# Performance work log

Hardware: AMD Instinct MI355X
Metric: run time of the kernel (lower is better)

## Reference

```python
import jax, jax.numpy as jnp
import numpy as np

TEMPERATURE = 0.1

def _l2norm(x):
    # F.normalize(dim=1) with eps clamp
    n = jnp.maximum(jnp.linalg.norm(x, axis=1, keepdims=True), 1e-12)
    return x / n

def _retrieval_metric(s):
    # T=1: position of the diagonal element in each row's descending sort.
    order = jnp.argsort(-s, axis=1)            # [N,N] descending argsort
    rankpos = jnp.argsort(order, axis=1)        # inverse permutation: rank of each column
    pos = jnp.diagonal(rankpos)                 # j such that rank[i][j] == i
    posf = pos.astype(s.dtype)
    r1 = jnp.mean((pos < 1).astype(s.dtype))
    r5 = jnp.mean((pos < 5).astype(s.dtype))
    r10 = jnp.mean((pos < 10).astype(s.dtype))
    mr = jnp.mean(posf)
    return r1, r5, r10, mr

def setup_inputs() -> dict:
    key = jax.random.key(0)
    k1, k2, k3, k4 = jax.random.split(key, 4)
    N, C = 4096, 512
    return {
        'v_feat': jax.random.normal(k1, (N, C), dtype=jnp.float32),
        't_feat': jax.random.normal(k2, (N, C), dtype=jnp.float32),
        'p_v': jax.random.normal(k3, (N, C), dtype=jnp.float32),
        'p_t': jax.random.normal(k4, (N, C), dtype=jnp.float32),
    }

def reference(v_feat, t_feat, p_v, p_t):
    vn = _l2norm(v_feat)
    tn = _l2norm(t_feat)
    pvn = _l2norm(p_v)
    ptn = _l2norm(p_t)
    sv = jnp.einsum('nc,mc->nm', vn, ptn) / TEMPERATURE  # [N,N]
    st = jnp.einsum('nc,mc->nm', tn, pvn) / TEMPERATURE  # [N,N]
    # nominator: scalar logsumexp over both diagonals (2N values)
    nominator = jax.nn.logsumexp(jnp.concatenate([jnp.diagonal(sv), jnp.diagonal(st)], axis=0))
    # denominator: per-row logsumexp over concatenated [N,2N]
    denominator = jax.nn.logsumexp(jnp.concatenate([sv, st], axis=1), axis=1)
    loss = jnp.mean(denominator - nominator)
    # metrics (no-grad path in original)
    v_std = jnp.mean(jnp.std(vn, axis=0, ddof=1))
    t_std = jnp.mean(jnp.std(tn, axis=0, ddof=1))
    pv_std = jnp.mean(jnp.std(pvn, axis=0, ddof=1))
    pt_std = jnp.mean(jnp.std(ptn, axis=0, ddof=1))
    sv_raw = jnp.einsum('nc,mc->nm', vn, ptn)
    st_raw = jnp.einsum('nc,mc->nm', tn, pvn)
    v_r1, v_r5, v_r10, v_mr = _retrieval_metric(sv_raw)
    t_r1, t_r5, t_r10, t_mr = _retrieval_metric(st_raw)
    return (loss, v_std, t_std, pv_std, pt_std,
            v_r1, v_r5, v_r10, v_mr,
            t_r1, t_r5, t_r10, t_mr)
```

## Files before the change

### kernel.cpp

```cpp
#include <hip/hip_runtime.h>
#include <hip/hip_bf16.h>

#define N 4096
#define C 512

typedef __attribute__((ext_vector_type(8))) short bf16x8;
typedef __attribute__((ext_vector_type(8))) short s16x8;
typedef __attribute__((ext_vector_type(4))) float f32x4;

__device__ inline float bf2f(__hip_bfloat16 h) { return __bfloat162float(h); }

__device__ inline void gload16(const void* g, void* l) {
    __builtin_amdgcn_global_load_lds(
        (__attribute__((address_space(1))) void*)(g),
        (__attribute__((address_space(3))) void*)(l),
        16, 0, 0);
}

__global__ __launch_bounds__(256) void k_prep(
    const float* __restrict__ s0, const float* __restrict__ s1f,
    const float* __restrict__ s2f, const float* __restrict__ s3,
    __hip_bfloat16* __restrict__ ws_hi0, long mat_stride,
    float* __restrict__ dv, float* __restrict__ dt,
    float* __restrict__ colsum, float* __restrict__ colsq)
{
    __shared__ float sa[4][512];
    __shared__ float sq[4][512];

    const int b = blockIdx.x;
    const int tid = threadIdx.x;
    const int lane = tid & 63;
    const int w = tid >> 6;

    const int pair = b >> 8;
    const int chunk = b & 255;
    const float* X = pair ? s1f : s0;
    const float* B = pair ? s2f : s3;
    const int mX = pair ? 1 : 0;
    const int mB = pair ? 2 : 3;
    __hip_bfloat16* hiX = ws_hi0 + (long)mX * mat_stride;
    __hip_bfloat16* loX = hiX + (long)N * C;
    __hip_bfloat16* hiB = ws_hi0 + (long)mB * mat_stride;
    __hip_bfloat16* loB = hiB + (long)N * C;
    float* dout = pair ? dt : dv;

    float aX[8], qX[8], aB[8], qB[8];
    for (int e = 0; e < 8; e++) { aX[e] = 0.f; qX[e] = 0.f; aB[e] = 0.f; qB[e] = 0.f; }

    const int row0 = chunk * 16 + w * 4;
    for (int i = 0; i < 4; i++) {
        const int row = row0 + i;
        const float4* x4 = (const float4*)(X + (size_t)row * C);
        const float4* b4 = (const float4*)(B + (size_t)row * C);
        float4 x0 = x4[lane * 2], x1 = x4[lane * 2 + 1];
        float4 b0 = b4[lane * 2], b1 = b4[lane * 2 + 1];

        float ss  = x0.x*x0.x + x0.y*x0.y + x0.z*x0.z + x0.w*x0.w
                  + x1.x*x1.x + x1.y*x1.y + x1.z*x1.z + x1.w*x1.w;
        float ssb = b0.x*b0.x + b0.y*b0.y + b0.z*b0.z + b0.w*b0.w
                  + b1.x*b1.x + b1.y*b1.y + b1.z*b1.z + b1.w*b1.w;
        float dot = x0.x*b0.x + x0.y*b0.y + x0.z*b0.z + x0.w*b0.w
                  + x1.x*b1.x + x1.y*b1.y + x1.z*b1.z + x1.w*b1.w;
        for (int o = 1; o < 64; o <<= 1) {
            ss  += __shfl_xor(ss, o);
            ssb += __shfl_xor(ssb, o);
            dot += __shfl_xor(dot, o);
        }
        float scX = 1.0f / fmaxf(sqrtf(ss), 1e-12f);
        float scB = 1.0f / fmaxf(sqrtf(ssb), 1e-12f);
        if (lane == 0) dout[row] = dot * scX * scB;

        float yx[8] = { x0.x*scX, x0.y*scX, x0.z*scX, x0.w*scX,
                        x1.x*scX, x1.y*scX, x1.z*scX, x1.w*scX };
        float yb[8] = { b0.x*scB, b0.y*scB, b0.z*scB, b0.w*scB,
                        b1.x*scB, b1.y*scB, b1.z*scB, b1.w*scB };
        __hip_bfloat16 hvx[8], lvx[8], hvb[8], lvb[8];
        for (int e = 0; e < 8; e++) {
            hvx[e] = __float2bfloat16(yx[e]);
            lvx[e] = __float2bfloat16(yx[e] - bf2f(hvx[e]));
            aX[e] += yx[e]; qX[e] += yx[e] * yx[e];
            hvb[e] = __float2bfloat16(yb[e]);
            lvb[e] = __float2bfloat16(yb[e] - bf2f(hvb[e]));
            aB[e] += yb[e]; qB[e] += yb[e] * yb[e];
        }
        size_t base = (size_t)row * C + lane * 8;
        *(s16x8*)(hiX + base) = *(s16x8*)hvx;
        *(s16x8*)(loX + base) = *(s16x8*)lvx;
        *(s16x8*)(hiB + base) = *(s16x8*)hvb;
        *(s16x8*)(loB + base) = *(s16x8*)lvb;
    }

    for (int e = 0; e < 8; e++) { sa[w][lane*8+e] = aX[e]; sq[w][lane*8+e] = qX[e]; }
    __syncthreads();
    for (int c = tid; c < 512; c += 256) {
        atomicAdd(&colsum[mX * 512 + c], sa[0][c] + sa[1][c] + sa[2][c] + sa[3][c]);
        atomicAdd(&colsq [mX * 512 + c], sq[0][c] + sq[1][c] + sq[2][c] + sq[3][c]);
    }
    __syncthreads();
    for (int e = 0; e < 8; e++) { sa[w][lane*8+e] = aB[e]; sq[w][lane*8+e] = qB[e]; }
    __syncthreads();
    for (int c = tid; c < 512; c += 256) {
        atomicAdd(&colsum[mB * 512 + c], sa[0][c] + sa[1][c] + sa[2][c] + sa[3][c]);
        atomicAdd(&colsq [mB * 512 + c], sq[0][c] + sq[1][c] + sq[2][c] + sq[3][c]);
    }
}

__global__ __launch_bounds__(256) void k_gemm(
    const __hip_bfloat16* __restrict__ h0, const __hip_bfloat16* __restrict__ l0,
    const __hip_bfloat16* __restrict__ h1, const __hip_bfloat16* __restrict__ l1,
    const __hip_bfloat16* __restrict__ h2, const __hip_bfloat16* __restrict__ l2,
    const __hip_bfloat16* __restrict__ h3, const __hip_bfloat16* __restrict__ l3,
    const float* __restrict__ dv, const float* __restrict__ dt,
    float* __restrict__ row_ev, float* __restrict__ row_et,
    float* __restrict__ row_cv, float* __restrict__ row_ct)
{
    __shared__ __align__(16) __hip_bfloat16 sA[2][128][32];
    __shared__ __align__(16) __hip_bfloat16 sB[2][128][32];
    __shared__ float sdiag[128];
    __shared__ float sred[128][2][2];

    const int z = blockIdx.z;
    const __hip_bfloat16* Ah = z ? h1 : h0;
    const __hip_bfloat16* Al = z ? l1 : l0;
    const __hip_bfloat16* Bh = z ? h2 : h3;
    const __hip_bfloat16* Bl = z ? l2 : l3;
    const float* diag = z ? dt : dv;
    float* row_e = z ? row_et : row_ev;
    float* row_c = z ? row_ct : row_cv;

    const int tid = threadIdx.x;
    const int lane = tid & 63;
    const int w = tid >> 6;
    const int wy = w >> 1, wx = w & 1;
    const int bm = blockIdx.x * 128;
    const int bn = blockIdx.y * 128;

    if (tid < 128) sdiag[tid] = diag[bm + tid];

    f32x4 acc[4][4];
    for (int i = 0; i < 4; i++)
        for (int j = 0; j < 4; j++)
            acc[i][j] = (f32x4){0.f, 0.f, 0.f, 0.f};

    const int srow = lane >> 2;
    const int lcol = (lane & 3) * 8;
    const int scolg = (((lane & 3) ^ ((lane >> 3) & 3))) * 8;
    const int fr = lane & 15;
    const int pcs = ((lane >> 4) ^ ((fr >> 1) & 3)) * 8;

    for (int k0 = 0; k0 < C; k0 += 32) {
        for (int half = 0; half < 2; half++) {
            int rr = w * 16 + half * 64 + srow;
            size_t ga = (size_t)(bm + rr) * C + k0 + scolg;
            size_t gb = (size_t)(bn + rr) * C + k0 + scolg;
            gload16(Ah + ga, &sA[0][rr][lcol]);
            gload16(Al + ga, &sA[1][rr][lcol]);
            gload16(Bh + gb, &sB[0][rr][lcol]);
            gload16(Bl + gb, &sB[1][rr][lcol]);
        }
        __syncthreads();

        bf16x8 a_h[4], a_l[4], b_h[4], b_l[4];
        for (int i = 0; i < 4; i++) {
            a_h[i] = *(const bf16x8*)&sA[0][wy * 64 + i * 16 + fr][pcs];
            a_l[i] = *(const bf16x8*)&sA[1][wy * 64 + i * 16 + fr][pcs];
            b_h[i] = *(const bf16x8*)&sB[0][wx * 64 + i * 16 + fr][pcs];
            b_l[i] = *(const bf16x8*)&sB[1][wx * 64 + i * 16 + fr][pcs];
        }
        for (int i = 0; i < 4; i++)
            for (int j = 0; j < 4; j++) {
                acc[i][j] = __builtin_amdgcn_mfma_f32_16x16x32_bf16(a_h[i], b_h[j], acc[i][j], 0, 0, 0);
                acc[i][j] = __builtin_amdgcn_mfma_f32_16x16x32_bf16(a_h[i], b_l[j], acc[i][j], 0, 0, 0);
                acc[i][j] = __builtin_amdgcn_mfma_f32_16x16x32_bf16(a_l[i], b_h[j], acc[i][j], 0, 0, 0);
            }
        __syncthreads();
    }

    const int quad = lane >> 4;
    for (int i = 0; i < 4; i++) {
        for (int reg = 0; reg < 4; reg++) {
            int rloc = wy * 64 + i * 16 + quad * 4 + reg;
            int grow = bm + rloc;
            float d = sdiag[rloc];
            float e = 0.f, c = 0.f;
            for (int j = 0; j < 4; j++) {
                float s = acc[i][j][reg];
                int gcol = bn + wx * 64 + j * 16 + fr;
                e += __expf(10.f * s - 10.f);
                if (s > d && gcol != grow) c += 1.f;
            }
            for (int o = 1; o < 16; o <<= 1) {
                e += __shfl_xor(e, o);
                c += __shfl_xor(c, o);
            }
            if (fr == 0) { sred[rloc][wx][0] = e; sred[rloc][wx][1] = c; }
        }
    }
    __syncthreads();
    if (tid < 128) {
        atomicAdd(&row_e[bm + tid], sred[tid][0][0] + sred[tid][1][0]);
        atomicAdd(&row_c[bm + tid], sred[tid][0][1] + sred[tid][1][1]);
    }
}

__global__ __launch_bounds__(256) void k_fin(
    const float* __restrict__ dv, const float* __restrict__ dt,
    const float* __restrict__ row_ev, const float* __restrict__ row_et,
    const float* __restrict__ row_cv, const float* __restrict__ row_ct,
    const float* __restrict__ colsum, const float* __restrict__ colsq,
    float* __restrict__ out)
{
    const int t = threadIdx.x;
    const int lane = t & 63;
    const int wv = t >> 6;

    float vals[10];
    for (int k = 0; k < 10; k++) vals[k] = 0.f;
    for (int i = 0; i < 16; i++) {
        const int row = i * 256 + t;
        float se = row_ev[row] + row_et[row];
        float pv = row_cv[row];
        float pt = row_ct[row];
        vals[0] += logf(se) + 10.f;
        vals[1] += (pv < 0.5f) ? 1.f : 0.f;
        vals[2] += (pv < 4.5f) ? 1.f : 0.f;
        vals[3] += (pv < 9.5f) ? 1.f : 0.f;
        vals[4] += pv;
        vals[5] += (pt < 0.5f) ? 1.f : 0.f;
        vals[6] += (pt < 4.5f) ? 1.f : 0.f;
        vals[7] += (pt < 9.5f) ? 1.f : 0.f;
        vals[8] += pt;
        vals[9] += __expf(10.f * dv[row] - 10.f) + __expf(10.f * dt[row] - 10.f);
    }
    __shared__ float red[4][10];
    for (int k = 0; k < 10; k++) {
        float v = vals[k];
        for (int o = 1; o < 64; o <<= 1) v += __shfl_xor(v, o);
        if (lane == 0) red[wv][k] = v;
    }

    __shared__ float smat[4][4];
    for (int m = 0; m < 4; m++) {
        float sd2 = 0.f;
        for (int h = 0; h < 2; h++) {
            int c = h * 256 + t;
            float a = colsum[m * 512 + c];
            float q = colsq [m * 512 + c];
            float var = (q - a * a * (1.f / N)) * (1.f / (N - 1));
            sd2 += sqrtf(fmaxf(var, 0.f));
        }
        for (int o = 1; o < 64; o <<= 1) sd2 += __shfl_xor(sd2, o);
        if (lane == 0) smat[wv][m] = sd2;
    }
    __syncthreads();
    if (t == 0) {
        float g[10];
        for (int k = 0; k < 10; k++)
            g[k] = red[0][k] + red[1][k] + red[2][k] + red[3][k];
        float stds[4];
        for (int m = 0; m < 4; m++)
            stds[m] = (smat[0][m] + smat[1][m] + smat[2][m] + smat[3][m]) * (1.f / 512.f);
        const float invN = 1.f / N;
        float nominator = logf(g[9]) + 10.f;
        out[0]  = g[0] * invN - nominator;
        out[1]  = stds[0];
        out[2]  = stds[1];
        out[3]  = stds[2];
        out[4]  = stds[3];
        out[5]  = g[1] * invN;
        out[6]  = g[2] * invN;
        out[7]  = g[3] * invN;
        out[8]  = g[4] * invN;
        out[9]  = g[5] * invN;
        out[10] = g[6] * invN;
        out[11] = g[7] * invN;
        out[12] = g[8] * invN;
    }
}

extern "C" void kernel_launch(void* const* d_in, const int* in_sizes, int n_in,
                              void* d_out, int out_size, void* d_ws, size_t ws_size,
                              hipStream_t stream)
{
    char* p = (char*)d_ws;

    float* row_ev = (float*)p; p += N * 4;
    float* row_et = (float*)p; p += N * 4;
    float* row_cv = (float*)p; p += N * 4;
    float* row_ct = (float*)p; p += N * 4;
    float* colsum = (float*)p; p += 4 * 512 * 4;
    float* colsq  = (float*)p; p += 4 * 512 * 4;
    const size_t acc_bytes = (size_t)(p - (char*)d_ws);

    const size_t NE = (size_t)N * C;
    const long mat_stride = 2 * NE;
    __hip_bfloat16* hiA[4];
    __hip_bfloat16* loA[4];
    for (int m = 0; m < 4; m++) {
        hiA[m] = (__hip_bfloat16*)p; p += NE * 2;
        loA[m] = (__hip_bfloat16*)p; p += NE * 2;
    }
    float* dv = (float*)p; p += N * 4;
    float* dt = (float*)p; p += N * 4;

    hipMemsetAsync(d_ws, 0, acc_bytes, stream);

    k_prep<<<dim3(512), 256, 0, stream>>>(
        (const float*)d_in[0], (const float*)d_in[1],
        (const float*)d_in[2], (const float*)d_in[3],
        hiA[0], mat_stride, dv, dt, colsum, colsq);

    k_gemm<<<dim3(32, 32, 2), 256, 0, stream>>>(
        hiA[0], loA[0], hiA[1], loA[1], hiA[2], loA[2], hiA[3], loA[3],
        dv, dt, row_ev, row_et, row_cv, row_ct);

    k_fin<<<dim3(1), 256, 0, stream>>>(
        dv, dt, row_ev, row_et, row_cv, row_ct, colsum, colsq, (float*)d_out);
}
```

Measured before the change: 214.9 us.

## Enlarge GEMM tiles to 256x256 with double-buffered LDS and interleaved prefetch

The split-bf16 similarity GEMM moves from 128x128 tiles with 256 threads to 256x256 tiles with 512 threads (8 waves). It uses a 128KB double-buffered shared-memory layout: loads for the next K-step are issued part-way through the current step's MFMA phases, and the MFMA phases are bracketed by explicit barriers and priority raises. This is meant to hide global-load latency and raise the arithmetic done per byte loaded. The cost is heavy LDS use that limits the GPU to about one block per CU, more accumulator registers, and fewer blocks to cover the machine.

```diff
diff --git a/kernel.cpp b/kernel.cpp
--- a/kernel.cpp
+++ b/kernel.cpp
@@ -105,7 +105,10 @@
     }
 }
 
-__global__ __launch_bounds__(256) void k_gemm(
+#define PLANE 8192
+#define LIDX(BUF, ROW, COL) ((BUF) * PLANE + (ROW) * 32 + (COL))
+
+__global__ __launch_bounds__(512, 2) void k_gemm(
     const __hip_bfloat16* __restrict__ h0, const __hip_bfloat16* __restrict__ l0,
     const __hip_bfloat16* __restrict__ h1, const __hip_bfloat16* __restrict__ l1,
     const __hip_bfloat16* __restrict__ h2, const __hip_bfloat16* __restrict__ l2,
@@ -114,10 +117,11 @@
     float* __restrict__ row_ev, float* __restrict__ row_et,
     float* __restrict__ row_cv, float* __restrict__ row_ct)
 {
-    __shared__ __align__(16) __hip_bfloat16 sA[2][128][32];
-    __shared__ __align__(16) __hip_bfloat16 sB[2][128][32];
-    __shared__ float sdiag[128];
-    __shared__ float sred[128][2][2];
+    __shared__ __align__(16) char smem[131072];
+    __hip_bfloat16* SAh = (__hip_bfloat16*)smem;
+    __hip_bfloat16* SAl = SAh + 2 * PLANE;
+    __hip_bfloat16* SBh = SAh + 4 * PLANE;
+    __hip_bfloat16* SBl = SAh + 6 * PLANE;
 
     const int z = blockIdx.z;
     const __hip_bfloat16* Ah = z ? h1 : h0;
@@ -131,75 +135,177 @@
     const int tid = threadIdx.x;
     const int lane = tid & 63;
     const int w = tid >> 6;
-    const int wy = w >> 1, wx = w & 1;
-    const int bm = blockIdx.x * 128;
-    const int bn = blockIdx.y * 128;
-
-    if (tid < 128) sdiag[tid] = diag[bm + tid];
-
-    f32x4 acc[4][4];
-    for (int i = 0; i < 4; i++)
+    const int wy = w >> 2, wx = w & 3;
+    const int bm = blockIdx.x * 256;
+    const int bn = blockIdx.y * 256;
+
+    const int s0i = tid, s1i = tid + 512;
+    const int r0 = s0i >> 2, q0 = s0i & 3;
+    const int r1 = s1i >> 2, q1 = s1i & 3;
+    const int g0 = (q0 ^ ((r0 >> 1) & 3)) * 8;
+    const int g1 = (q1 ^ ((r1 >> 1) & 3)) * 8;
+    const size_t aoff0 = (size_t)(bm + r0) * C + g0;
+    const size_t aoff1 = (size_t)(bm + r1) * C + g1;
+    const size_t boff0 = (size_t)(bn + r0) * C + g0;
+    const size_t boff1 = (size_t)(bn + r1) * C + g1;
+    const int d0 = s0i * 8, d1 = s1i * 8;
+
+    const int fr = lane & 15;
+    const int pcs = ((lane >> 4) ^ ((fr >> 1) & 3)) * 8;
+
+    f32x4 acc[8][4];
+    #pragma unroll
+    for (int i = 0; i < 8; i++)
+        #pragma unroll
         for (int j = 0; j < 4; j++)
             acc[i][j] = (f32x4){0.f, 0.f, 0.f, 0.f};
 
-    const int srow = lane >> 2;
-    const int lcol = (lane & 3) * 8;
-    const int scolg = (((lane & 3) ^ ((lane >> 3) & 3))) * 8;
-    const int fr = lane & 15;
-    const int pcs = ((lane >> 4) ^ ((fr >> 1) & 3)) * 8;
-
-    for (int k0 = 0; k0 < C; k0 += 32) {
-        for (int half = 0; half < 2; half++) {
-            int rr = w * 16 + half * 64 + srow;
-            size_t ga = (size_t)(bm + rr) * C + k0 + scolg;
-            size_t gb = (size_t)(bn + rr) * C + k0 + scolg;
-            gload16(Ah + ga, &sA[0][rr][lcol]);
-            gload16(Al + ga, &sA[1][rr][lcol]);
-            gload16(Bh + gb, &sB[0][rr][lcol]);
-            gload16(Bl + gb, &sB[1][rr][lcol]);
-        }
-        __syncthreads();
-
-        bf16x8 a_h[4], a_l[4], b_h[4], b_l[4];
-        for (int i = 0; i < 4; i++) {
-            a_h[i] = *(const bf16x8*)&sA[0][wy * 64 + i * 16 + fr][pcs];
-            a_l[i] = *(const bf16x8*)&sA[1][wy * 64 + i * 16 + fr][pcs];
-            b_h[i] = *(const bf16x8*)&sB[0][wx * 64 + i * 16 + fr][pcs];
-            b_l[i] = *(const bf16x8*)&sB[1][wx * 64 + i * 16 + fr][pcs];
-        }
-        for (int i = 0; i < 4; i++)
-            for (int j = 0; j < 4; j++) {
-                acc[i][j] = __builtin_amdgcn_mfma_f32_16x16x32_bf16(a_h[i], b_h[j], acc[i][j], 0, 0, 0);
-                acc[i][j] = __builtin_amdgcn_mfma_f32_16x16x32_bf16(a_h[i], b_l[j], acc[i][j], 0, 0, 0);
-                acc[i][j] = __builtin_amdgcn_mfma_f32_16x16x32_bf16(a_l[i], b_h[j], acc[i][j], 0, 0, 0);
-            }
-        __syncthreads();
-    }
+    gload16(Ah + aoff0, SAh + d0); gload16(Ah + aoff1, SAh + d1);
+    gload16(Al + aoff0, SAl + d0); gload16(Al + aoff1, SAl + d1);
+    gload16(Bh + boff0, SBh + d0); gload16(Bh + boff1, SBh + d1);
+    gload16(Bl + boff0, SBl + d0); gload16(Bl + boff1, SBl + d1);
+    __syncthreads();
+
+#define MFMA1(d, a, b) d = __builtin_amdgcn_mfma_f32_16x16x32_bf16(a, b, d, 0, 0, 0)
+#define QUAD(i0, i1, A0H, A0L, A1H, A1L) \
+    MFMA1(acc[i0][0], A0H, bh[0]); MFMA1(acc[i0][1], A0H, bh[1]); \
+    MFMA1(acc[i0][2], A0H, bh[2]); MFMA1(acc[i0][3], A0H, bh[3]); \
+    MFMA1(acc[i1][0], A1H, bh[0]); MFMA1(acc[i1][1], A1H, bh[1]); \
+    MFMA1(acc[i1][2], A1H, bh[2]); MFMA1(acc[i1][3], A1H, bh[3]); \
+    MFMA1(acc[i0][0], A0H, bl[0]); MFMA1(acc[i0][1], A0H, bl[1]); \
+    MFMA1(acc[i0][2], A0H, bl[2]); MFMA1(acc[i0][3], A0H, bl[3]); \
+    MFMA1(acc[i1][0], A1H, bl[0]); MFMA1(acc[i1][1], A1H, bl[1]); \
+    MFMA1(acc[i1][2], A1H, bl[2]); MFMA1(acc[i1][3], A1H, bl[3]); \
+    MFMA1(acc[i0][0], A0L, bh[0]); MFMA1(acc[i0][1], A0L, bh[1]); \
+    MFMA1(acc[i0][2], A0L, bh[2]); MFMA1(acc[i0][3], A0L, bh[3]); \
+    MFMA1(acc[i1][0], A1L, bh[0]); MFMA1(acc[i1][1], A1L, bh[1]); \
+    MFMA1(acc[i1][2], A1L, bh[2]); MFMA1(acc[i1][3], A1L, bh[3])
+
+#define KBODY(RB, TCUR)                                                          \
+    {                                                                            \
+        const size_t kn = (size_t)((TCUR) + 1) * 32;                             \
+        const int fpl = (1 - (RB)) * PLANE;                                      \
+        const bool pf = ((TCUR) < NT - 1);                                       \
+        bf16x8 bh[4], bl[4];                                                     \
+        {                    \
+            _Pragma("unroll")                                                    \
+            for (int j = 0; j < 4; j++) {                                        \
+                bh[j] = *(const bf16x8*)&SBh[LIDX(RB, wx*64 + j*16 + fr, pcs)];  \
+                bl[j] = *(const bf16x8*)&SBl[LIDX(RB, wx*64 + j*16 + fr, pcs)];  \
+            }                                                                    \
+            bf16x8 x0h = *(const bf16x8*)&SAh[LIDX(RB, wy*128 +   0 + fr, pcs)]; \
+            bf16x8 x0l = *(const bf16x8*)&SAl[LIDX(RB, wy*128 +   0 + fr, pcs)]; \
+            bf16x8 x1h = *(const bf16x8*)&SAh[LIDX(RB, wy*128 +  16 + fr, pcs)]; \
+            bf16x8 x1l = *(const bf16x8*)&SAl[LIDX(RB, wy*128 +  16 + fr, pcs)]; \
+            if (pf) {                                                            \
+                gload16(Ah + aoff0 + kn, SAh + fpl + d0);                        \
+                gload16(Ah + aoff1 + kn, SAh + fpl + d1);                        \
+                gload16(Al + aoff0 + kn, SAl + fpl + d0);                        \
+                gload16(Al + aoff1 + kn, SAl + fpl + d1);                        \
+            }                                                                    \
+            __builtin_amdgcn_s_barrier();                                        \
+            asm volatile("s_waitcnt lgkmcnt(0)" ::: "memory");                   \
+            __builtin_amdgcn_s_setprio(1);                                       \
+            QUAD(0, 1, x0h, x0l, x1h, x1l);                                      \
+            __builtin_amdgcn_s_setprio(0);                                       \
+            __builtin_amdgcn_s_barrier();                                        \
+        }                                                                        \
+        {                              \
+            bf16x8 x0h = *(const bf16x8*)&SAh[LIDX(RB, wy*128 +  32 + fr, pcs)]; \
+            bf16x8 x0l = *(const bf16x8*)&SAl[LIDX(RB, wy*128 +  32 + fr, pcs)]; \
+            bf16x8 x1h = *(const bf16x8*)&SAh[LIDX(RB, wy*128 +  48 + fr, pcs)]; \
+            bf16x8 x1l = *(const bf16x8*)&SAl[LIDX(RB, wy*128 +  48 + fr, pcs)]; \
+            if (pf) {                                                            \
+                gload16(Bh + boff0 + kn, SBh + fpl + d0);                        \
+                gload16(Bh + boff1 + kn, SBh + fpl + d1);                        \
+                gload16(Bl + boff0 + kn, SBl + fpl + d0);                        \
+                gload16(Bl + boff1 + kn, SBl + fpl + d1);                        \
+            }                                                                    \
+            __builtin_amdgcn_s_barrier();                                        \
+            asm volatile("s_waitcnt lgkmcnt(0)" ::: "memory");                   \
+            __builtin_amdgcn_s_setprio(1);                                       \
+            QUAD(2, 3, x0h, x0l, x1h, x1l);                                      \
+            __builtin_amdgcn_s_setprio(0);                                       \
+            __builtin_amdgcn_s_barrier();                                        \
+        }                                                                        \
+        {                                                  \
+            bf16x8 x0h = *(const bf16x8*)&SAh[LIDX(RB, wy*128 +  64 + fr, pcs)]; \
+            bf16x8 x0l = *(const bf16x8*)&SAl[LIDX(RB, wy*128 +  64 + fr, pcs)]; \
+            bf16x8 x1h = *(const bf16x8*)&SAh[LIDX(RB, wy*128 +  80 + fr, pcs)]; \
+            bf16x8 x1l = *(const bf16x8*)&SAl[LIDX(RB, wy*128 +  80 + fr, pcs)]; \
+            __builtin_amdgcn_s_barrier();                                        \
+            asm volatile("s_waitcnt lgkmcnt(0)" ::: "memory");                   \
+            __builtin_amdgcn_s_setprio(1);                                       \
+            QUAD(4, 5, x0h, x0l, x1h, x1l);                                      \
+            __builtin_amdgcn_s_setprio(0);                                       \
+            __builtin_amdgcn_s_barrier();                                        \
+        }                                                                        \
+        {                           \
+            bf16x8 x0h = *(const bf16x8*)&SAh[LIDX(RB, wy*128 +  96 + fr, pcs)]; \
+            bf16x8 x0l = *(const bf16x8*)&SAl[LIDX(RB, wy*128 +  96 + fr, pcs)]; \
+            bf16x8 x1h = *(const bf16x8*)&SAh[LIDX(RB, wy*128 + 112 + fr, pcs)]; \
+            bf16x8 x1l = *(const bf16x8*)&SAl[LIDX(RB, wy*128 + 112 + fr, pcs)]; \
+            __builtin_amdgcn_s_barrier();                                        \
+            asm volatile("s_waitcnt lgkmcnt(0)" ::: "memory");                   \
+            __builtin_amdgcn_s_setprio(1);                                       \
+            QUAD(6, 7, x0h, x0l, x1h, x1l);                                      \
+            __builtin_amdgcn_s_setprio(0);                                       \
+            asm volatile("s_waitcnt vmcnt(0)" ::: "memory");                     \
+            __builtin_amdgcn_s_barrier();                                        \
+        }                                                                        \
+    }
+
+    const int NT = C / 32;
+    #pragma unroll 1
+    for (int tt = 0; tt < NT; tt += 2) {
+        KBODY(0, tt)
+        KBODY(1, tt + 1)
+    }
+#undef KBODY
+#undef QUAD
+#undef MFMA1
+
+    float* sdiag = (float*)smem;
+    float* sred  = (float*)(smem + 1024);
+    if (tid < 256) sdiag[tid] = diag[bm + tid];
+    __syncthreads();
 
     const int quad = lane >> 4;
-    for (int i = 0; i < 4; i++) {
+    #pragma unroll
+    for (int i = 0; i < 8; i++) {
+        #pragma unroll
         for (int reg = 0; reg < 4; reg++) {
-            int rloc = wy * 64 + i * 16 + quad * 4 + reg;
-            int grow = bm + rloc;
-            float d = sdiag[rloc];
-            float e = 0.f, c = 0.f;
+            const int rloc = wy * 128 + i * 16 + quad * 4 + reg;
+            const int grow = bm + rloc;
+            const float dgv = sdiag[rloc];
+            float e = 0.f, cc = 0.f;
+            #pragma unroll
             for (int j = 0; j < 4; j++) {
                 float s = acc[i][j][reg];
                 int gcol = bn + wx * 64 + j * 16 + fr;
                 e += __expf(10.f * s - 10.f);
-                if (s > d && gcol != grow) c += 1.f;
+                if (s > dgv && gcol != grow) cc += 1.f;
             }
             for (int o = 1; o < 16; o <<= 1) {
                 e += __shfl_xor(e, o);
-                c += __shfl_xor(c, o);
+                cc += __shfl_xor(cc, o);
             }
-            if (fr == 0) { sred[rloc][wx][0] = e; sred[rloc][wx][1] = c; }
+            if (fr == 0) {
+                sred[(rloc * 4 + wx) * 2 + 0] = e;
+                sred[(rloc * 4 + wx) * 2 + 1] = cc;
+            }
         }
     }
     __syncthreads();
-    if (tid < 128) {
-        atomicAdd(&row_e[bm + tid], sred[tid][0][0] + sred[tid][1][0]);
-        atomicAdd(&row_c[bm + tid], sred[tid][0][1] + sred[tid][1][1]);
+    if (tid < 256) {
+        float se = 0.f, sc = 0.f;
+        #pragma unroll
+        for (int x = 0; x < 4; x++) {
+            se += sred[(tid * 4 + x) * 2 + 0];
+            sc += sred[(tid * 4 + x) * 2 + 1];
+        }
+        atomicAdd(&row_e[bm + tid], se);
+        atomicAdd(&row_c[bm + tid], sc);
     }
 }
 
@@ -310,7 +416,7 @@
         (const float*)d_in[2], (const float*)d_in[3],
         hiA[0], mat_stride, dv, dt, colsum, colsq);
 
-    k_gemm<<<dim3(32, 32, 2), 256, 0, stream>>>(
+    k_gemm<<<dim3(16, 16, 2), 512, 0, stream>>>(
         hiA[0], loA[0], hiA[1], loA[1], hiA[2], loA[2], hiA[3], loA[3],
         dv, dt, row_ev, row_et, row_cv, row_ct);
 
```

Result: faster. 191.2 us (-11.0%).
